# Kernel optimization log

Hardware: AMD Instinct MI355X
Metric: run time of the kernel (lower is better)

The kernel has to match this reference:

```python
import jax, jax.numpy as jnp
import numpy as np

B, S, D, H = 2, 2048, 1024, 16
HD = D // H
EPS = 1e-5


def setup_inputs() -> dict:
    key = jax.random.key(0)
    ks = jax.random.split(key, 8)
    std = 1.0 / np.sqrt(D)
    x = jax.random.normal(ks[0], (B, S, D), dtype=jnp.float32)
    # causal mask: True = attend (masked_fill where mask==0)
    attention_mask = jnp.tril(jnp.ones((S, S), dtype=bool))[None, None].repeat(B, axis=0)
    return {
        "x": x,
        "attention_mask": attention_mask,
        "ln_gamma": jnp.ones((D,), jnp.float32),
        "ln_beta": jnp.zeros((D,), jnp.float32),
        "w_qkv": jax.random.uniform(ks[1], (D, 3 * D), jnp.float32, -std, std),
        "b_qkv": jnp.zeros((3 * D,), jnp.float32),
        "w_gate": jax.random.uniform(ks[2], (D, D), jnp.float32, -std, std),
        "b_gate": jnp.zeros((D,), jnp.float32),
        "w_out": jax.random.uniform(ks[3], (D, D), jnp.float32, -std, std),
        "b_out": jnp.zeros((D,), jnp.float32),
        "rel_pos_bias": jnp.zeros((1, H, 1, 1), jnp.float32),
    }


def reference(x, attention_mask, ln_gamma, ln_beta, w_qkv, b_qkv,
              w_gate, b_gate, w_out, b_out, rel_pos_bias):
    # LayerNorm over model dim
    mu = jnp.mean(x, axis=-1, keepdims=True)
    var = jnp.mean(jnp.square(x - mu), axis=-1, keepdims=True)
    xn = (x - mu) * jax.lax.rsqrt(var + EPS) * ln_gamma + ln_beta

    qkv = xn @ w_qkv + b_qkv                      # [B,S,3D]
    qkv = qkv.reshape(B, S, 3, H, HD)
    q = qkv[:, :, 0].transpose(0, 2, 1, 3)        # [B,H,S,HD]
    k = qkv[:, :, 1].transpose(0, 2, 1, 3)
    v = qkv[:, :, 2].transpose(0, 2, 1, 3)

    u = jax.nn.silu(xn @ w_gate + b_gate)         # [B,S,D] SiLU gate

    scale = HD ** -0.5
    scores = jnp.einsum('bhqd,bhkd->bhqk', q * scale, k) + rel_pos_bias
    # masked_fill(mask==0, -inf) then sigmoid == zero out masked entries
    attn = jnp.where(attention_mask, jax.nn.sigmoid(scores), 0.0)
    ctx = jnp.einsum('bhqk,bhkd->bhqd', attn, v)  # [B,H,S,HD]
    ctx = ctx.transpose(0, 2, 1, 3).reshape(B, S, D)

    out = (ctx * u) @ w_out + b_out               # gated output proj
    return x + out                                # dropout=eval identity
```

## Files before the change

### kernel.cpp

```cpp
#include <hip/hip_runtime.h>
#include <hip/hip_bf16.h>
#include <cmath>

#define BB 2
#define SS 2048
#define DD 1024
#define HH 16
#define EPS 1e-5f
#define LOG2E 1.44269504088896f
#define QSCALE (0.125f * LOG2E)

typedef __attribute__((ext_vector_type(8))) short short8;
typedef __attribute__((ext_vector_type(4))) float f32x4;

__device__ inline unsigned short f2bf(float f) {
  union { float f; unsigned int u; } v; v.f = f;
  unsigned int u = v.u;
  unsigned int r = (u + 0x7FFFu + ((u >> 16) & 1u)) >> 16;
  return (unsigned short)r;
}
__device__ inline float bf2f(unsigned short h) {
  union { unsigned int u; float f; } v; v.u = ((unsigned int)h) << 16;
  return v.f;
}
__device__ inline unsigned short f2bf_fast(float f) {
  union { float f; unsigned int u; } v; v.f = f;
  return (unsigned short)((v.u + 0x8000u) >> 16);
}

__global__ __launch_bounds__(256) void ln_kernel(
    const float* __restrict__ x, const float* __restrict__ gamma,
    const float* __restrict__ beta, unsigned short* __restrict__ xn) {
  int row = blockIdx.x;
  int t = threadIdx.x;
  const float* xr = x + (size_t)row * DD;
  float4 v = *(const float4*)(xr + t * 4);
  float s = v.x + v.y + v.z + v.w;
  float sq = v.x * v.x + v.y * v.y + v.z * v.z + v.w * v.w;
  for (int off = 32; off > 0; off >>= 1) {
    s += __shfl_down(s, off, 64);
    sq += __shfl_down(sq, off, 64);
  }
  __shared__ float ls[4], lq[4];
  int wave = t >> 6, lane = t & 63;
  if (lane == 0) { ls[wave] = s; lq[wave] = sq; }
  __syncthreads();
  float tot = ls[0] + ls[1] + ls[2] + ls[3];
  float totq = lq[0] + lq[1] + lq[2] + lq[3];
  float mu = tot * (1.0f / DD);
  float var = totq * (1.0f / DD) - mu * mu;
  float rstd = rsqrtf(var + EPS);
  float4 g = *(const float4*)(gamma + t * 4);
  float4 bt = *(const float4*)(beta + t * 4);
  ushort4 o;
  o.x = f2bf((v.x - mu) * rstd * g.x + bt.x);
  o.y = f2bf((v.y - mu) * rstd * g.y + bt.y);
  o.z = f2bf((v.z - mu) * rstd * g.z + bt.z);
  o.w = f2bf((v.w - mu) * rstd * g.w + bt.w);
  *(ushort4*)(xn + (size_t)row * DD + t * 4) = o;
}

__global__ __launch_bounds__(256) void wtrans(
    const float* __restrict__ W, unsigned short* __restrict__ Wt,
    int K, int N) {
  __shared__ unsigned short tile[32][33];
  int bx = blockIdx.x * 32;
  int by = blockIdx.y * 32;
  int tx = threadIdx.x & 31, ty = threadIdx.x >> 5;
#pragma unroll
  for (int i = 0; i < 32; i += 8)
    tile[ty + i][tx] = f2bf(W[(size_t)(by + ty + i) * N + bx + tx]);
  __syncthreads();
#pragma unroll
  for (int i = 0; i < 32; i += 8)
    Wt[(size_t)(bx + ty + i) * K + by + tx] = tile[tx][ty + i];
}

__global__ __launch_bounds__(256) void gemm_qkvg(
    const unsigned short* __restrict__ A, const unsigned short* __restrict__ Bt,
    const float* __restrict__ bqkv, const float* __restrict__ bgate,
    unsigned short* __restrict__ qkb, unsigned short* __restrict__ vTb,
    unsigned short* __restrict__ ub) {
  __shared__ unsigned short As[128 * 32];
  __shared__ unsigned short Bs[128 * 32];
  const int K = 1024;
  int tid = threadIdx.x;
  int wave = tid >> 6, lane = tid & 63;
  int quad = lane >> 4, m16 = lane & 15;
  int wm = wave >> 1, wn = wave & 1;
  int m0 = blockIdx.y * 128, n0 = blockIdx.x * 128;

  int lrow = tid >> 2;
  int lcol = (tid & 3) * 8;
  const unsigned short* Ar0 = A + (size_t)(m0 + lrow) * K + lcol;
  const unsigned short* Ar1 = A + (size_t)(m0 + lrow + 64) * K + lcol;
  const unsigned short* Br0 = Bt + (size_t)(n0 + lrow) * K + lcol;
  const unsigned short* Br1 = Bt + (size_t)(n0 + lrow + 64) * K + lcol;

  f32x4 acc[4][4];
#pragma unroll
  for (int i = 0; i < 4; ++i)
#pragma unroll
    for (int j = 0; j < 4; ++j) acc[i][j] = (f32x4){0.f, 0.f, 0.f, 0.f};

  uint4 a0 = *(const uint4*)Ar0;
  uint4 a1 = *(const uint4*)Ar1;
  uint4 b0 = *(const uint4*)Br0;
  uint4 b1 = *(const uint4*)Br1;

  for (int k0 = 0; k0 < K; k0 += 32) {
    __syncthreads();
    *(uint4*)&As[lrow * 32 + lcol] = a0;
    *(uint4*)&As[(lrow + 64) * 32 + lcol] = a1;
    *(uint4*)&Bs[lrow * 32 + lcol] = b0;
    *(uint4*)&Bs[(lrow + 64) * 32 + lcol] = b1;
    __syncthreads();
    if (k0 + 32 < K) {
      a0 = *(const uint4*)(Ar0 + k0 + 32);
      a1 = *(const uint4*)(Ar1 + k0 + 32);
      b0 = *(const uint4*)(Br0 + k0 + 32);
      b1 = *(const uint4*)(Br1 + k0 + 32);
    }
    short8 af[4], bfr[4];
#pragma unroll
    for (int mi = 0; mi < 4; ++mi)
      af[mi] = *(const short8*)&As[(wm * 64 + mi * 16 + m16) * 32 + quad * 8];
#pragma unroll
    for (int ni = 0; ni < 4; ++ni)
      bfr[ni] = *(const short8*)&Bs[(wn * 64 + ni * 16 + m16) * 32 + quad * 8];
#pragma unroll
    for (int mi = 0; mi < 4; ++mi)
#pragma unroll
      for (int ni = 0; ni < 4; ++ni)
        acc[mi][ni] = __builtin_amdgcn_mfma_f32_16x16x32_bf16(
            af[mi], bfr[ni], acc[mi][ni], 0, 0, 0);
  }

  int nwin = n0 + wn * 64;
  int sec = nwin >> 10;
  if (sec <= 1) {
    float qs = (sec == 0) ? QSCALE : 1.0f;
#pragma unroll
    for (int ni = 0; ni < 4; ++ni) {
      int col = nwin + ni * 16 + m16;
      float bb = bqkv[col];
#pragma unroll
      for (int mi = 0; mi < 4; ++mi)
#pragma unroll
        for (int r = 0; r < 4; ++r) {
          int row = m0 + wm * 64 + mi * 16 + quad * 4 + r;
          qkb[(size_t)row * 2048 + col] = f2bf((acc[mi][ni][r] + bb) * qs);
        }
    }
  } else if (sec == 2) {
#pragma unroll
    for (int ni = 0; ni < 4; ++ni) {
      int col = nwin + ni * 16 + m16;
      float bb = bqkv[col];
      int vcol = col - 2048;
      int hh = vcol >> 6, dd = vcol & 63;
#pragma unroll
      for (int mi = 0; mi < 4; ++mi) {
        int row0 = m0 + wm * 64 + mi * 16 + quad * 4;
        int bat = row0 >> 11, s0 = row0 & 2047;
        ushort4 o;
        o.x = f2bf(acc[mi][ni][0] + bb);
        o.y = f2bf(acc[mi][ni][1] + bb);
        o.z = f2bf(acc[mi][ni][2] + bb);
        o.w = f2bf(acc[mi][ni][3] + bb);
        *(ushort4*)&vTb[(size_t)((bat * 16 + hh) * 64 + dd) * 2048 + s0] = o;
      }
    }
  } else {
#pragma unroll
    for (int ni = 0; ni < 4; ++ni) {
      int col = nwin + ni * 16 + m16;
      int g = col - 3072;
      float bb = bgate[g];
#pragma unroll
      for (int mi = 0; mi < 4; ++mi)
#pragma unroll
        for (int r = 0; r < 4; ++r) {
          int row = m0 + wm * 64 + mi * 16 + quad * 4 + r;
          float v = acc[mi][ni][r] + bb;
          v = v * __builtin_amdgcn_rcpf(1.0f + exp2f(-v * LOG2E));
          ub[(size_t)row * 1024 + g] = f2bf(v);
        }
    }
  }
}

__global__ __launch_bounds__(256) void gemm_out(
    const unsigned short* __restrict__ A, const unsigned short* __restrict__ Bt,
    const float* __restrict__ bias, const float* __restrict__ resid,
    float* __restrict__ C) {
  __shared__ unsigned short As[128 * 32];
  __shared__ unsigned short Bs[128 * 32];
  const int K = 1024, N = 1024;
  int tid = threadIdx.x;
  int wave = tid >> 6, lane = tid & 63;
  int quad = lane >> 4, m16 = lane & 15;
  int wm = wave >> 1, wn = wave & 1;
  int m0 = blockIdx.y * 128, n0 = blockIdx.x * 128;
  int lrow = tid >> 2;
  int lcol = (tid & 3) * 8;
  const unsigned short* Ar0 = A + (size_t)(m0 + lrow) * K + lcol;
  const unsigned short* Ar1 = A + (size_t)(m0 + lrow + 64) * K + lcol;
  const unsigned short* Br0 = Bt + (size_t)(n0 + lrow) * K + lcol;
  const unsigned short* Br1 = Bt + (size_t)(n0 + lrow + 64) * K + lcol;

  f32x4 acc[4][4];
#pragma unroll
  for (int i = 0; i < 4; ++i)
#pragma unroll
    for (int j = 0; j < 4; ++j) acc[i][j] = (f32x4){0.f, 0.f, 0.f, 0.f};

  uint4 a0 = *(const uint4*)Ar0;
  uint4 a1 = *(const uint4*)Ar1;
  uint4 b0 = *(const uint4*)Br0;
  uint4 b1 = *(const uint4*)Br1;

  for (int k0 = 0; k0 < K; k0 += 32) {
    __syncthreads();
    *(uint4*)&As[lrow * 32 + lcol] = a0;
    *(uint4*)&As[(lrow + 64) * 32 + lcol] = a1;
    *(uint4*)&Bs[lrow * 32 + lcol] = b0;
    *(uint4*)&Bs[(lrow + 64) * 32 + lcol] = b1;
    __syncthreads();
    if (k0 + 32 < K) {
      a0 = *(const uint4*)(Ar0 + k0 + 32);
      a1 = *(const uint4*)(Ar1 + k0 + 32);
      b0 = *(const uint4*)(Br0 + k0 + 32);
      b1 = *(const uint4*)(Br1 + k0 + 32);
    }
    short8 af[4], bfr[4];
#pragma unroll
    for (int mi = 0; mi < 4; ++mi)
      af[mi] = *(const short8*)&As[(wm * 64 + mi * 16 + m16) * 32 + quad * 8];
#pragma unroll
    for (int ni = 0; ni < 4; ++ni)
      bfr[ni] = *(const short8*)&Bs[(wn * 64 + ni * 16 + m16) * 32 + quad * 8];
#pragma unroll
    for (int mi = 0; mi < 4; ++mi)
#pragma unroll
      for (int ni = 0; ni < 4; ++ni)
        acc[mi][ni] = __builtin_amdgcn_mfma_f32_16x16x32_bf16(
            af[mi], bfr[ni], acc[mi][ni], 0, 0, 0);
  }
#pragma unroll
  for (int ni = 0; ni < 4; ++ni) {
    int col = n0 + wn * 64 + ni * 16 + m16;
    float bb = bias[col];
#pragma unroll
    for (int mi = 0; mi < 4; ++mi)
#pragma unroll
      for (int r = 0; r < 4; ++r) {
        int row = m0 + wm * 64 + mi * 16 + quad * 4 + r;
        C[(size_t)row * N + col] =
            acc[mi][ni][r] + bb + resid[(size_t)row * N + col];
      }
  }
}

__global__ __launch_bounds__(256) void attn_mfma(
    const unsigned short* __restrict__ qk, const unsigned short* __restrict__ vT,
    const unsigned short* __restrict__ u, const float* __restrict__ rpb,
    unsigned short* __restrict__ prod) {
  __shared__ unsigned short Qs[128 * 72];
  __shared__ unsigned short Ks[64 * 72];
  __shared__ unsigned short Vs[64 * 72];
  __shared__ unsigned short Ps[64 * 72];

  int qtA = blockIdx.x;
  int qtB = 31 - qtA;
  int q0A = qtA * 64, q0B = qtB * 64;
  int bh = blockIdx.y;
  int b = bh >> 4, h = bh & 15;
  int t = threadIdx.x;
  int wave = t >> 6, lane = t & 63;
  int quad = lane >> 4, m16 = lane & 15;

  const unsigned short* qbase = qk + (size_t)(b * SS) * 2048 + h * 64;
  const unsigned short* kbase = qbase + 1024;
  const unsigned short* vbase = vT + (size_t)bh * 64 * 2048;

  int row = t >> 3, blk8 = (t & 7) * 8;

  {
    const unsigned short* sA = qbase + (size_t)(q0A + row) * 2048 + blk8;
    const unsigned short* sB = qbase + (size_t)(q0B + row) * 2048 + blk8;
    *(uint4*)&Qs[row * 72 + blk8] = *(const uint4*)sA;
    *(uint4*)&Qs[(row + 32) * 72 + blk8] = *(const uint4*)(sA + (size_t)32 * 2048);
    *(uint4*)&Qs[(row + 64) * 72 + blk8] = *(const uint4*)sB;
    *(uint4*)&Qs[(row + 96) * 72 + blk8] = *(const uint4*)(sB + (size_t)32 * 2048);
  }

  f32x4 zero4 = {0.f, 0.f, 0.f, 0.f};
  f32x4 caccA[4], caccB[4];
#pragma unroll
  for (int nb = 0; nb < 4; ++nb) { caccA[nb] = zero4; caccB[nb] = zero4; }

  float hb2 = rpb[h] * LOG2E;
  int ktmax = qtB;

  for (int kt = 0; kt <= ktmax; ++kt) {
    int k0 = kt * 64;
    const unsigned short* kp = kbase + (size_t)(k0 + row) * 2048 + blk8;
    const unsigned short* vp = vbase + (size_t)row * 2048 + k0 + blk8;
    uint4 kv0 = *(const uint4*)kp;
    uint4 kv1 = *(const uint4*)(kp + (size_t)32 * 2048);
    uint4 vv0 = *(const uint4*)vp;
    uint4 vv1 = *(const uint4*)(vp + (size_t)32 * 2048);
    __syncthreads();
    *(uint4*)&Ks[row * 72 + blk8] = kv0;
    *(uint4*)&Ks[(row + 32) * 72 + blk8] = kv1;
    *(uint4*)&Vs[row * 72 + blk8] = vv0;
    *(uint4*)&Vs[(row + 32) * 72 + blk8] = vv1;
    __syncthreads();

#pragma unroll
    for (int tile = 0; tile < 2; ++tile) {
      if (tile == 1 && kt > qtA) break;
      int qlds = (tile == 0) ? (64 + wave * 16) : (wave * 16);
      int q0 = (tile == 0) ? q0B : q0A;
      bool diag = (tile == 0) ? (kt == qtB) : (kt == qtA);
      f32x4* cacc = (tile == 0) ? caccB : caccA;

      f32x4 sacc[4];
#pragma unroll
      for (int nb = 0; nb < 4; ++nb) sacc[nb] = zero4;
#pragma unroll
      for (int s = 0; s < 2; ++s) {
        short8 a = *(const short8*)&Qs[(qlds + m16) * 72 + s * 32 + quad * 8];
#pragma unroll
        for (int nb = 0; nb < 4; ++nb) {
          short8 bf = *(const short8*)&Ks[(nb * 16 + m16) * 72 + s * 32 + quad * 8];
          sacc[nb] = __builtin_amdgcn_mfma_f32_16x16x32_bf16(a, bf, sacc[nb], 0, 0, 0);
        }
      }
#pragma unroll
      for (int nb = 0; nb < 4; ++nb) {
#pragma unroll
        for (int r = 0; r < 4; ++r) {
          float y = sacc[nb][r] + hb2;
          float p = __builtin_amdgcn_rcpf(1.0f + exp2f(-y));
          if (diag) {
            int key = k0 + nb * 16 + m16;
            int q = q0 + wave * 16 + quad * 4 + r;
            if (key > q) p = 0.f;
          }
          Ps[(wave * 16 + quad * 4 + r) * 72 + nb * 16 + m16] = f2bf_fast(p);
        }
      }
#pragma unroll
      for (int s = 0; s < 2; ++s) {
        short8 a = *(const short8*)&Ps[(wave * 16 + m16) * 72 + s * 32 + quad * 8];
#pragma unroll
        for (int nb = 0; nb < 4; ++nb) {
          short8 bf = *(const short8*)&Vs[(nb * 16 + m16) * 72 + s * 32 + quad * 8];
          cacc[nb] = __builtin_amdgcn_mfma_f32_16x16x32_bf16(a, bf, cacc[nb], 0, 0, 0);
        }
      }
    }
  }

  const unsigned short* ub_ = u + (size_t)(b * SS) * 1024 + h * 64;
  unsigned short* pb_ = prod + (size_t)(b * SS) * 1024 + h * 64;
#pragma unroll
  for (int nb = 0; nb < 4; ++nb) {
    int d = nb * 16 + m16;
#pragma unroll
    for (int r = 0; r < 4; ++r) {
      int qA = q0A + wave * 16 + quad * 4 + r;
      int qB = q0B + wave * 16 + quad * 4 + r;
      pb_[(size_t)qA * 1024 + d] = f2bf(caccA[nb][r] * bf2f(ub_[(size_t)qA * 1024 + d]));
      pb_[(size_t)qB * 1024 + d] = f2bf(caccB[nb][r] * bf2f(ub_[(size_t)qB * 1024 + d]));
    }
  }
}

extern "C" void kernel_launch(void* const* d_in, const int* in_sizes, int n_in,
                              void* d_out, int out_size, void* d_ws, size_t ws_size,
                              hipStream_t stream) {
  const float* x      = (const float*)d_in[0];
  const float* gamma  = (const float*)d_in[2];
  const float* beta   = (const float*)d_in[3];
  const float* w_qkv  = (const float*)d_in[4];
  const float* b_qkv  = (const float*)d_in[5];
  const float* w_gate = (const float*)d_in[6];
  const float* b_gate = (const float*)d_in[7];
  const float* w_out  = (const float*)d_in[8];
  const float* b_out  = (const float*)d_in[9];
  const float* rpb    = (const float*)d_in[10];
  float* out = (float*)d_out;

  unsigned short* xnb   = (unsigned short*)d_ws;
  unsigned short* qkb   = xnb + 4194304;
  unsigned short* vTb   = qkb + 8388608;
  unsigned short* ub    = vTb + 4194304;
  unsigned short* prodb = ub + 4194304;
  unsigned short* wcatT = prodb + 4194304;
  unsigned short* woutT = wcatT + 4194304;

  ln_kernel<<<BB * SS, 256, 0, stream>>>(x, gamma, beta, xnb);
  wtrans<<<dim3(3072 / 32, 1024 / 32), 256, 0, stream>>>(w_qkv, wcatT, 1024, 3072);
  wtrans<<<dim3(1024 / 32, 1024 / 32), 256, 0, stream>>>(w_gate, wcatT + (size_t)3072 * 1024, 1024, 1024);
  wtrans<<<dim3(1024 / 32, 1024 / 32), 256, 0, stream>>>(w_out, woutT, 1024, 1024);
  gemm_qkvg<<<dim3(4096 / 128, 4096 / 128), 256, 0, stream>>>(
      xnb, wcatT, b_qkv, b_gate, qkb, vTb, ub);
  attn_mfma<<<dim3(16, BB * HH), 256, 0, stream>>>(qkb, vTb, ub, rpb, prodb);
  gemm_out<<<dim3(1024 / 128, 4096 / 128), 256, 0, stream>>>(
      prodb, woutT, b_out, x, out);
}
```

Baseline: 254.2 us.

## Merge weight transposes, stage V-transpose via LDS, hoist K/V fragments, swizzle P

Merges the three weight-transpose launches into a single kernel. The V-section epilogue of the QKV GEMM now stages the tile through swizzled shared memory, so it can write coalesced 16-byte rows into the transposed V buffer instead of scattered 8-byte stores. In the attention kernel, K/V MFMA fragments are loaded from LDS once per key tile and reused across both query tiles, and the P scratch buffer gets an XOR swizzle to cut bank conflicts. The changes add extra barriers in the epilogue and more registers held in attention, which may lower occupancy.

```diff
diff --git a/kernel.cpp b/kernel.cpp
--- a/kernel.cpp
+++ b/kernel.cpp
@@ -60,20 +60,27 @@
   *(ushort4*)(xn + (size_t)row * DD + t * 4) = o;
 }
 
-__global__ __launch_bounds__(256) void wtrans(
-    const float* __restrict__ W, unsigned short* __restrict__ Wt,
-    int K, int N) {
+__global__ __launch_bounds__(256) void wtrans_all(
+    const float* __restrict__ wq, const float* __restrict__ wg,
+    const float* __restrict__ wo, unsigned short* __restrict__ wcatT,
+    unsigned short* __restrict__ woutT) {
   __shared__ unsigned short tile[32][33];
-  int bx = blockIdx.x * 32;
+  int bx = blockIdx.x;
+  const float* W;
+  unsigned short* Wt;
+  int N, colbase;
+  if (bx < 96)       { W = wq; Wt = wcatT; N = 3072; colbase = bx * 32; }
+  else if (bx < 128) { W = wg; Wt = wcatT + (size_t)3072 * 1024; N = 1024; colbase = (bx - 96) * 32; }
+  else               { W = wo; Wt = woutT; N = 1024; colbase = (bx - 128) * 32; }
   int by = blockIdx.y * 32;
   int tx = threadIdx.x & 31, ty = threadIdx.x >> 5;
 #pragma unroll
   for (int i = 0; i < 32; i += 8)
-    tile[ty + i][tx] = f2bf(W[(size_t)(by + ty + i) * N + bx + tx]);
+    tile[ty + i][tx] = f2bf(W[(size_t)(by + ty + i) * N + colbase + tx]);
   __syncthreads();
 #pragma unroll
   for (int i = 0; i < 32; i += 8)
-    Wt[(size_t)(bx + ty + i) * K + by + tx] = tile[tx][ty + i];
+    Wt[(size_t)(colbase + ty + i) * 1024 + by + tx] = tile[tx][ty + i];
 }
 
 __global__ __launch_bounds__(256) void gemm_qkvg(
@@ -81,8 +88,9 @@
     const float* __restrict__ bqkv, const float* __restrict__ bgate,
     unsigned short* __restrict__ qkb, unsigned short* __restrict__ vTb,
     unsigned short* __restrict__ ub) {
-  __shared__ unsigned short As[128 * 32];
-  __shared__ unsigned short Bs[128 * 32];
+  __shared__ unsigned short SH[128 * 64];
+  unsigned short* As = SH;
+  unsigned short* Bs = SH + 128 * 32;
   const int K = 1024;
   int tid = threadIdx.x;
   int wave = tid >> 6, lane = tid & 63;
@@ -136,56 +144,73 @@
             af[mi], bfr[ni], acc[mi][ni], 0, 0, 0);
   }
 
-  int nwin = n0 + wn * 64;
-  int sec = nwin >> 10;
-  if (sec <= 1) {
-    float qs = (sec == 0) ? QSCALE : 1.0f;
-#pragma unroll
-    for (int ni = 0; ni < 4; ++ni) {
-      int col = nwin + ni * 16 + m16;
-      float bb = bqkv[col];
-#pragma unroll
-      for (int mi = 0; mi < 4; ++mi)
-#pragma unroll
-        for (int r = 0; r < 4; ++r) {
-          int row = m0 + wm * 64 + mi * 16 + quad * 4 + r;
-          qkb[(size_t)row * 2048 + col] = f2bf((acc[mi][ni][r] + bb) * qs);
+  int sec = n0 >> 10;
+  if (sec == 2) {
+    int bat = m0 >> 11;
+    int s_base = m0 & 2047;
+    int dgbase = n0 - 2048;
+#pragma unroll
+    for (int p = 0; p < 2; ++p) {
+      __syncthreads();
+      if (wn == p) {
+#pragma unroll
+        for (int ni = 0; ni < 4; ++ni) {
+          int dl = ni * 16 + m16;
+          float bb = bqkv[2048 + dgbase + p * 64 + dl];
+#pragma unroll
+          for (int mi = 0; mi < 4; ++mi)
+#pragma unroll
+            for (int r = 0; r < 4; ++r) {
+              int sl = wm * 64 + mi * 16 + quad * 4 + r;
+              int sls = sl ^ ((dl & 7) << 4);
+              SH[dl * 128 + sls] = f2bf(acc[mi][ni][r] + bb);
+            }
         }
-    }
-  } else if (sec == 2) {
-#pragma unroll
-    for (int ni = 0; ni < 4; ++ni) {
-      int col = nwin + ni * 16 + m16;
-      float bb = bqkv[col];
-      int vcol = col - 2048;
-      int hh = vcol >> 6, dd = vcol & 63;
-#pragma unroll
-      for (int mi = 0; mi < 4; ++mi) {
-        int row0 = m0 + wm * 64 + mi * 16 + quad * 4;
-        int bat = row0 >> 11, s0 = row0 & 2047;
-        ushort4 o;
-        o.x = f2bf(acc[mi][ni][0] + bb);
-        o.y = f2bf(acc[mi][ni][1] + bb);
-        o.z = f2bf(acc[mi][ni][2] + bb);
-        o.w = f2bf(acc[mi][ni][3] + bb);
-        *(ushort4*)&vTb[(size_t)((bat * 16 + hh) * 64 + dd) * 2048 + s0] = o;
+      }
+      __syncthreads();
+      int dl = tid >> 2;
+      int dg = dgbase + p * 64 + dl;
+      unsigned short* dst =
+          vTb + ((size_t)(bat * 16 + (dg >> 6)) * 64 + (dg & 63)) * 2048 + s_base;
+#pragma unroll
+      for (int i = 0; i < 4; ++i) {
+        int s0 = (tid & 3) * 8 + i * 32;
+        int s0s = s0 ^ ((dl & 7) << 4);
+        *(uint4*)(dst + s0) = *(const uint4*)&SH[dl * 128 + s0s];
       }
     }
   } else {
-#pragma unroll
-    for (int ni = 0; ni < 4; ++ni) {
-      int col = nwin + ni * 16 + m16;
-      int g = col - 3072;
-      float bb = bgate[g];
-#pragma unroll
-      for (int mi = 0; mi < 4; ++mi)
-#pragma unroll
-        for (int r = 0; r < 4; ++r) {
-          int row = m0 + wm * 64 + mi * 16 + quad * 4 + r;
-          float v = acc[mi][ni][r] + bb;
-          v = v * __builtin_amdgcn_rcpf(1.0f + exp2f(-v * LOG2E));
-          ub[(size_t)row * 1024 + g] = f2bf(v);
-        }
+    int nwin = n0 + wn * 64;
+    if (sec <= 1) {
+      float qs = (sec == 0) ? QSCALE : 1.0f;
+#pragma unroll
+      for (int ni = 0; ni < 4; ++ni) {
+        int col = nwin + ni * 16 + m16;
+        float bb = bqkv[col];
+#pragma unroll
+        for (int mi = 0; mi < 4; ++mi)
+#pragma unroll
+          for (int r = 0; r < 4; ++r) {
+            int row = m0 + wm * 64 + mi * 16 + quad * 4 + r;
+            qkb[(size_t)row * 2048 + col] = f2bf((acc[mi][ni][r] + bb) * qs);
+          }
+      }
+    } else {
+#pragma unroll
+      for (int ni = 0; ni < 4; ++ni) {
+        int col = nwin + ni * 16 + m16;
+        int g = col - 3072;
+        float bb = bgate[g];
+#pragma unroll
+        for (int mi = 0; mi < 4; ++mi)
+#pragma unroll
+          for (int r = 0; r < 4; ++r) {
+            int row = m0 + wm * 64 + mi * 16 + quad * 4 + r;
+            float v = acc[mi][ni][r] + bb;
+            v = v * __builtin_amdgcn_rcpf(1.0f + exp2f(-v * LOG2E));
+            ub[(size_t)row * 1024 + g] = f2bf(v);
+          }
+      }
     }
   }
 }
@@ -302,6 +327,8 @@
 
   float hb2 = rpb[h] * LOG2E;
   int ktmax = qtB;
+  int psw = quad << 3;
+  int psr = ((m16 >> 2) & 3) << 3;
 
   for (int kt = 0; kt <= ktmax; ++kt) {
     int k0 = kt * 64;
@@ -318,6 +345,15 @@
     *(uint4*)&Vs[(row + 32) * 72 + blk8] = vv1;
     __syncthreads();
 
+    short8 kf[2][4], vf[2][4];
+#pragma unroll
+    for (int s = 0; s < 2; ++s)
+#pragma unroll
+      for (int nb = 0; nb < 4; ++nb) {
+        kf[s][nb] = *(const short8*)&Ks[(nb * 16 + m16) * 72 + s * 32 + quad * 8];
+        vf[s][nb] = *(const short8*)&Vs[(nb * 16 + m16) * 72 + s * 32 + quad * 8];
+      }
+
 #pragma unroll
     for (int tile = 0; tile < 2; ++tile) {
       if (tile == 1 && kt > qtA) break;
@@ -333,10 +369,8 @@
       for (int s = 0; s < 2; ++s) {
         short8 a = *(const short8*)&Qs[(qlds + m16) * 72 + s * 32 + quad * 8];
 #pragma unroll
-        for (int nb = 0; nb < 4; ++nb) {
-          short8 bf = *(const short8*)&Ks[(nb * 16 + m16) * 72 + s * 32 + quad * 8];
-          sacc[nb] = __builtin_amdgcn_mfma_f32_16x16x32_bf16(a, bf, sacc[nb], 0, 0, 0);
-        }
+        for (int nb = 0; nb < 4; ++nb)
+          sacc[nb] = __builtin_amdgcn_mfma_f32_16x16x32_bf16(a, kf[s][nb], sacc[nb], 0, 0, 0);
       }
 #pragma unroll
       for (int nb = 0; nb < 4; ++nb) {
@@ -349,17 +383,17 @@
             int q = q0 + wave * 16 + quad * 4 + r;
             if (key > q) p = 0.f;
           }
-          Ps[(wave * 16 + quad * 4 + r) * 72 + nb * 16 + m16] = f2bf_fast(p);
+          int colS = (nb * 16 + m16) ^ psw;
+          Ps[(wave * 16 + quad * 4 + r) * 72 + colS] = f2bf_fast(p);
         }
       }
 #pragma unroll
       for (int s = 0; s < 2; ++s) {
-        short8 a = *(const short8*)&Ps[(wave * 16 + m16) * 72 + s * 32 + quad * 8];
-#pragma unroll
-        for (int nb = 0; nb < 4; ++nb) {
-          short8 bf = *(const short8*)&Vs[(nb * 16 + m16) * 72 + s * 32 + quad * 8];
-          cacc[nb] = __builtin_amdgcn_mfma_f32_16x16x32_bf16(a, bf, cacc[nb], 0, 0, 0);
-        }
+        int pcol = (s * 32 + quad * 8) ^ psr;
+        short8 a = *(const short8*)&Ps[(wave * 16 + m16) * 72 + pcol];
+#pragma unroll
+        for (int nb = 0; nb < 4; ++nb)
+          cacc[nb] = __builtin_amdgcn_mfma_f32_16x16x32_bf16(a, vf[s][nb], cacc[nb], 0, 0, 0);
       }
     }
   }
@@ -403,9 +437,7 @@
   unsigned short* woutT = wcatT + 4194304;
 
   ln_kernel<<<BB * SS, 256, 0, stream>>>(x, gamma, beta, xnb);
-  wtrans<<<dim3(3072 / 32, 1024 / 32), 256, 0, stream>>>(w_qkv, wcatT, 1024, 3072);
-  wtrans<<<dim3(1024 / 32, 1024 / 32), 256, 0, stream>>>(w_gate, wcatT + (size_t)3072 * 1024, 1024, 1024);
-  wtrans<<<dim3(1024 / 32, 1024 / 32), 256, 0, stream>>>(w_out, woutT, 1024, 1024);
+  wtrans_all<<<dim3(160, 32), 256, 0, stream>>>(w_qkv, w_gate, w_out, wcatT, woutT);
   gemm_qkvg<<<dim3(4096 / 128, 4096 / 128), 256, 0, stream>>>(
       xnb, wcatT, b_qkv, b_gate, qkb, vTb, ub);
   attn_mfma<<<dim3(16, BB * HH), 256, 0, stream>>>(qkb, vTb, ub, rpb, prodb);
```

Measured after the change: 251.1 us. About the same (-1.2%).
